# Performance work log

Measured on AMD Instinct MI355X. Metric: run time of the kernel, lower is better.

## Reference

```python
import jax, jax.numpy as jnp
import numpy as np
from jax import lax

B, S, D = 4, 4096, 2048
R, E, K, H = 256, 8, 2, 512
MAX_BLEND = 0.9


def setup_inputs() -> dict:
    key = jax.random.key(0)
    ks = jax.random.split(key, 11)
    def w(k, shape, fan_in):
        return jax.random.normal(k, shape, dtype=jnp.float32) * (1.0 / np.sqrt(fan_in))
    return {
        "h": jax.random.normal(ks[0], (B, S, D), dtype=jnp.float32),
        "V": w(ks[1], (D, R), D),            # down-projection (z = V^T h)
        "U": w(ks[2], (R, D), R),            # reconstruction (h = U z)
        "Wr": w(ks[3], (R, E), R),           # router
        "br": jnp.zeros((E,), dtype=jnp.float32),
        "W1": w(ks[4], (E, R, H), R),        # per-expert up-proj
        "b1": jnp.zeros((E, H), dtype=jnp.float32),
        "W2": w(ks[5], (E, H, R), H),        # per-expert down-proj
        "b2": jnp.zeros((E, R), dtype=jnp.float32),
        "Wh": w(ks[6], (D, 1), D),           # halting unit
        "bh": jnp.zeros((1,), dtype=jnp.float32),
    }


def _forward(h, V, U, Wr, br, W1, b1, W2, b2, Wh, bh):
    b, s, d = h.shape
    T = b * s
    # 1. project to vein subspace: z = V^T h  -> [B,S,R]
    z = jnp.einsum("bsd,dr->bsr", h, V)
    zf = z.reshape(T, R)
    # 2. top-k routing
    logits = zf @ Wr + br                      # [T,E]
    probs = jax.nn.softmax(logits, axis=-1)
    topw, topi = lax.top_k(probs, K)           # [T,K]
    topw = topw / jnp.sum(topw, axis=-1, keepdims=True)
    combine = jnp.zeros((T, E), dtype=zf.dtype).at[jnp.arange(T)[:, None], topi].add(topw)
    # 3. expert mix (dense-compute reference; combine is K-sparse per token)
    hidden = jax.nn.gelu(jnp.einsum("tr,erh->teh", zf, W1) + b1, approximate=False)
    expert_out = jnp.einsum("teh,ehr->ter", hidden, W2) + b2    # [T,E,R]
    z_new = jnp.einsum("te,ter->tr", combine, expert_out).reshape(b, s, R)
    # 4. residual blend: blend = min(top_k/num_experts, max_blend)
    blend = min(K / E, MAX_BLEND)
    z_final = z_new * blend + z * (1.0 - blend)
    # 5. reconstruct + halting
    h_new = jnp.einsum("bsr,rd->bsd", z_final, U)
    p_halt = jax.nn.sigmoid(jnp.einsum("bsd,do->bso", h_new, Wh) + bh)
    return h_new, p_halt


def reference(h, V, U, Wr, br, W1, b1, W2, b2, Wh, bh):
    return _forward(h, V, U, Wr, br, W1, b1, W2, b2, Wh, bh)
```

## Files before the change

### kernel.cpp

```cpp
#include <hip/hip_runtime.h>
#include <stdint.h>
#include <math.h>

#define TK 16384
#define DD 2048
#define RR 256
#define EE 8
#define HH 512
#define NSEG_MAX 264
#define NPAIR_MAX (NSEG_MAX * 128)

typedef __attribute__((ext_vector_type(4))) float f32x4;
typedef __attribute__((ext_vector_type(8))) short s16x8;
typedef __attribute__((ext_vector_type(8))) unsigned short u16x8;
typedef __attribute__((ext_vector_type(4))) unsigned short u16x4;
typedef unsigned short ushort_t;

__device__ inline unsigned short f2bf(float f) {
  union { float f; unsigned u; } v; v.f = f;
  unsigned r = v.u + 0x7fffu + ((v.u >> 16) & 1u);
  return (unsigned short)(r >> 16);
}
__device__ inline float bf2f(ushort_t u) {
  union { unsigned u; float f; } v; v.u = ((unsigned)u) << 16; return v.f;
}

__device__ inline void gll16(const void* g, void* l) {
  __builtin_amdgcn_global_load_lds(
      (const __attribute__((address_space(1))) void*)g,
      (__attribute__((address_space(3))) void*)l, 16, 0, 0);
}

__device__ inline u16x8 pack8(f32x4 a, f32x4 b) {
  u16x8 r;
  r[0] = f2bf(a.x); r[1] = f2bf(a.y); r[2] = f2bf(a.z); r[3] = f2bf(a.w);
  r[4] = f2bf(b.x); r[5] = f2bf(b.y); r[6] = f2bf(b.z); r[7] = f2bf(b.w);
  return r;
}

__global__ __launch_bounds__(256) void k_tr(const float* __restrict__ src,
                                            ushort_t* __restrict__ dst,
                                            int nr, int nc) {
  __shared__ float tile[32][33];
  int s = blockIdx.z;
  src += (size_t)s * nr * nc;
  dst += (size_t)s * nr * nc;
  int tx = threadIdx.x & 31, ty = threadIdx.x >> 5;
  int c0 = blockIdx.x * 32, r0 = blockIdx.y * 32;
  #pragma unroll
  for (int i = 0; i < 32; i += 8)
    tile[ty + i][tx] = src[(size_t)(r0 + ty + i) * nc + c0 + tx];
  __syncthreads();
  #pragma unroll
  for (int i = 0; i < 32; i += 8)
    dst[(size_t)(c0 + ty + i) * nr + r0 + tx] = f2bf(tile[tx][ty + i]);
}

__global__ __launch_bounds__(256) void k_veff(const float* __restrict__ V,
                                              const float* __restrict__ Wr,
                                              float* __restrict__ VeffT) {
  __shared__ float lwr[RR * EE];
  int t = threadIdx.x;
  #pragma unroll
  for (int i = 0; i < 8; ++i) lwr[i * 256 + t] = Wr[i * 256 + t];
  __syncthreads();
  int d = blockIdx.x * 256 + t;
  float a[8] = {0, 0, 0, 0, 0, 0, 0, 0};
  const float* vrow = V + (size_t)d * RR;
  for (int r = 0; r < RR; r += 4) {
    f32x4 v = *(const f32x4*)(vrow + r);
    #pragma unroll
    for (int e = 0; e < 8; ++e)
      a[e] += v.x * lwr[r * 8 + e] + v.y * lwr[(r + 1) * 8 + e] +
              v.z * lwr[(r + 2) * 8 + e] + v.w * lwr[(r + 3) * 8 + e];
  }
  #pragma unroll
  for (int e = 0; e < 8; ++e) VeffT[(size_t)e * DD + d] = a[e];
}

__global__ void k_uh(const float* U, const float* Wh, float* Uh) {
  int wave = threadIdx.x >> 6, lane = threadIdx.x & 63;
  int r = blockIdx.x * 4 + wave;
  const f32x4* u4 = (const f32x4*)(U + (size_t)r * DD);
  const f32x4* w4 = (const f32x4*)Wh;
  float acc = 0.f;
  #pragma unroll
  for (int it = 0; it < 8; ++it) {
    f32x4 a = u4[it * 64 + lane], b = w4[it * 64 + lane];
    acc += a.x * b.x + a.y * b.y + a.z * b.z + a.w * b.w;
  }
  #pragma unroll
  for (int o = 32; o; o >>= 1) acc += __shfl_down(acc, o, 64);
  if (lane == 0) Uh[r] = acc;
}

__global__ __launch_bounds__(256, 2) void k_front(
    const float* __restrict__ h, const ushort_t* __restrict__ Vt,
    const float* __restrict__ VeffT, const float* __restrict__ br,
    ushort_t* __restrict__ zb, int* __restrict__ topi, float* __restrict__ topw,
    int* __restrict__ ctrl) {
  __shared__ ushort_t As[2][32 * 72];
  __shared__ ushort_t Bs[2][256 * 64];
  __shared__ float Vs[2][8 * 64];
  __shared__ int lcnt[8];
  int t = threadIdx.x;
  int m0 = blockIdx.x * 32;
  int lane = t & 63, wave = t >> 6;
  int ln = lane & 15, hi = lane >> 4;
  int arow = t >> 3, koff = (t & 7) * 8;
  const float* aptr = h + (size_t)(m0 + arow) * DD + koff;
  if (t < 8) lcnt[t] = 0;

  f32x4 acc[2][4];
  #pragma unroll
  for (int i = 0; i < 2; ++i)
    #pragma unroll
    for (int j = 0; j < 4; ++j) acc[i][j] = (f32x4){0.f, 0.f, 0.f, 0.f};
  float racc[8] = {0, 0, 0, 0, 0, 0, 0, 0};

  f32x4 pc0, pc1, pn0, pn1;
  {
    pc0 = ((const f32x4*)aptr)[0];
    pc1 = ((const f32x4*)aptr)[1];
    #pragma unroll
    for (int u = 0; u < 8; ++u) {
      int idx = u * 256 + t;
      gll16(Vt + (size_t)(idx >> 3) * DD + (idx & 7) * 8, &Bs[0][idx * 8]);
    }
    if (t < 128) gll16(VeffT + (size_t)(t >> 4) * DD + (t & 15) * 4, &Vs[0][t * 4]);
    *(u16x8*)&As[0][arow * 72 + koff] = pack8(pc0, pc1);
  }
  __syncthreads();

  for (int s = 0; s < 32; ++s) {
    int cb = s & 1, xb = cb ^ 1;
    int k1 = (s + 1) * 64;
    if (s < 31) {
      pn0 = ((const f32x4*)(aptr + k1))[0];
      pn1 = ((const f32x4*)(aptr + k1))[1];
      #pragma unroll
      for (int u = 0; u < 8; ++u) {
        int idx = u * 256 + t;
        gll16(Vt + (size_t)(idx >> 3) * DD + k1 + (idx & 7) * 8, &Bs[xb][idx * 8]);
      }
      if (t < 128) gll16(VeffT + (size_t)(t >> 4) * DD + k1 + (t & 15) * 4, &Vs[xb][t * 4]);
    }
    {
      const f32x4* vsb = (const f32x4*)&Vs[cb][0];
      #pragma unroll
      for (int e = 0; e < 8; ++e) {
        f32x4 v0 = vsb[(e * 64 + koff) >> 2];
        f32x4 v1 = vsb[((e * 64 + koff) >> 2) + 1];
        racc[e] += pc0.x * v0.x + pc0.y * v0.y + pc0.z * v0.z + pc0.w * v0.w +
                   pc1.x * v1.x + pc1.y * v1.y + pc1.z * v1.z + pc1.w * v1.w;
      }
    }
    #pragma unroll
    for (int ks = 0; ks < 2; ++ks) {
      s16x8 af[2], bq[4];
      #pragma unroll
      for (int i = 0; i < 2; ++i)
        af[i] = *(const s16x8*)&As[cb][(i * 16 + ln) * 72 + ks * 32 + hi * 8];
      #pragma unroll
      for (int j = 0; j < 4; ++j)
        bq[j] = *(const s16x8*)&Bs[cb][(wave * 64 + j * 16 + ln) * 64 + ks * 32 + hi * 8];
      #pragma unroll
      for (int i = 0; i < 2; ++i)
        #pragma unroll
        for (int j = 0; j < 4; ++j)
          acc[i][j] = __builtin_amdgcn_mfma_f32_16x16x32_bf16(af[i], bq[j], acc[i][j], 0, 0, 0);
    }
    if (s < 31) {
      *(u16x8*)&As[xb][arow * 72 + koff] = pack8(pn0, pn1);
      pc0 = pn0; pc1 = pn1;
    }
    __syncthreads();
  }

  #pragma unroll
  for (int i = 0; i < 2; ++i)
    #pragma unroll
    for (int j = 0; j < 4; ++j)
      #pragma unroll
      for (int r = 0; r < 4; ++r) {
        int row = m0 + i * 16 + hi * 4 + r;
        int col = wave * 64 + j * 16 + ln;
        zb[(size_t)row * RR + col] = f2bf(acc[i][j][r]);
      }

  #pragma unroll
  for (int e = 0; e < 8; ++e) {
    racc[e] += __shfl_xor(racc[e], 1, 64);
    racc[e] += __shfl_xor(racc[e], 2, 64);
    racc[e] += __shfl_xor(racc[e], 4, 64);
  }
  if ((t & 7) == 0) {
    int token = m0 + arow;
    f32x4 br0 = ((const f32x4*)br)[0], br1 = ((const f32x4*)br)[1];
    float l[8] = {racc[0] + br0.x, racc[1] + br0.y, racc[2] + br0.z, racc[3] + br0.w,
                  racc[4] + br1.x, racc[5] + br1.y, racc[6] + br1.z, racc[7] + br1.w};
    float best = -1e30f; int bi = 0;
    #pragma unroll
    for (int e = 0; e < 8; ++e) if (l[e] > best) { best = l[e]; bi = e; }
    float sec = -1e30f; int si = 0;
    #pragma unroll
    for (int e = 0; e < 8; ++e) if (e != bi && l[e] > sec) { sec = l[e]; si = e; }
    float w0 = 1.f / (1.f + expf(sec - best));
    topi[token * 2 + 0] = bi; topi[token * 2 + 1] = si;
    topw[token * 2 + 0] = w0; topw[token * 2 + 1] = 1.f - w0;
    atomicAdd(&lcnt[bi], 1);
    atomicAdd(&lcnt[si], 1);
  }
  __syncthreads();
  if (t < 8) atomicAdd(&ctrl[t], lcnt[t]);
}

__global__ void k_bases(int* ctrl) {
  if (threadIdx.x == 0) {
    int cum = 0;
    for (int e = 0; e < 8; ++e) {
      int c = ctrl[e];
      int segs = (c + 127) >> 7;
      ctrl[8 + e] = cum;
      for (int s2 = 0; s2 < segs; ++s2) ctrl[16 + (cum >> 7) + s2] = e;
      cum += segs << 7;
    }
    for (int s2 = cum >> 7; s2 < NSEG_MAX; ++s2) ctrl[16 + s2] = -1;
  }
}

__global__ __launch_bounds__(256) void k_scatter(const int* topi, const float* topw,
                                                 int* ctrl, int* pair_t, float* pair_w,
                                                 int* inv) {
  __shared__ int lcnt[8], lbase[8];
  int t = threadIdx.x;
  if (t < 8) lcnt[t] = 0;
  __syncthreads();
  int slot = blockIdx.x * 256 + t;
  int e = topi[slot];
  float wv = topw[slot];
  int lp = atomicAdd(&lcnt[e], 1);
  __syncthreads();
  if (t < 8) lbase[t] = atomicAdd(&ctrl[8 + t], lcnt[t]);
  __syncthreads();
  int p = lbase[e] + lp;
  pair_t[p] = slot >> 1;
  pair_w[p] = wv;
  inv[slot] = p;
}

#define GEMM_COMPUTE(AS, BS)                                                          \
  _Pragma("unroll")                                                                   \
  for (int ks = 0; ks < 2; ++ks) {                                                    \
    s16x8 af[4], bq[4];                                                               \
    _Pragma("unroll")                                                                 \
    for (int i = 0; i < 4; ++i)                                                       \
      af[i] = *(const s16x8*)&AS[(wr * 64 + i * 16 + ln) * 64 + ks * 32 + hi * 8];    \
    _Pragma("unroll")                                                                 \
    for (int j = 0; j < 4; ++j)                                                       \
      bq[j] = *(const s16x8*)&BS[(wc * 64 + j * 16 + ln) * 64 + ks * 32 + hi * 8];    \
    _Pragma("unroll")                                                                 \
    for (int i = 0; i < 4; ++i)                                                       \
      _Pragma("unroll")                                                               \
      for (int j = 0; j < 4; ++j)                                                     \
        acc[i][j] = __builtin_amdgcn_mfma_f32_16x16x32_bf16(af[i], bq[j], acc[i][j], 0, 0, 0); \
  }

__global__ __launch_bounds__(256, 2) void k_e1(const ushort_t* zb, const ushort_t* W1t,
                                               const float* b1, const int* ctrl,
                                               const int* pair_t, ushort_t* hidden) {
  __shared__ ushort_t As[2][8192];
  __shared__ ushort_t Bs[2][8192];
  __shared__ int pt[128];
  int sg = blockIdx.x >> 2, nt = blockIdx.x & 3;
  int e = ctrl[16 + sg];
  if (e < 0) return;
  int t = threadIdx.x;
  if (t < 128) pt[t] = pair_t[sg * 128 + t];
  __syncthreads();
  int n0 = nt * 128;
  const ushort_t* Bbase = W1t + (size_t)e * HH * RR;
  int lane = t & 63, wave = t >> 6;
  int wr = wave >> 1, wc = wave & 1;
  int ln = lane & 15, hi = lane >> 4;

  f32x4 acc[4][4];
  #pragma unroll
  for (int i = 0; i < 4; ++i)
    #pragma unroll
    for (int j = 0; j < 4; ++j) acc[i][j] = (f32x4){0.f, 0.f, 0.f, 0.f};

  #pragma unroll
  for (int u = 0; u < 4; ++u) {
    int idx = u * 256 + t;
    gll16(zb + (size_t)pt[idx >> 3] * RR + (idx & 7) * 8, &As[0][idx * 8]);
    gll16(Bbase + (size_t)(n0 + (idx >> 3)) * RR + (idx & 7) * 8, &Bs[0][idx * 8]);
  }
  __syncthreads();
  for (int s = 0; s < 4; ++s) {
    int cb = s & 1, xb = cb ^ 1;
    if (s < 3) {
      int k1 = (s + 1) * 64;
      #pragma unroll
      for (int u = 0; u < 4; ++u) {
        int idx = u * 256 + t;
        gll16(zb + (size_t)pt[idx >> 3] * RR + k1 + (idx & 7) * 8, &As[xb][idx * 8]);
        gll16(Bbase + (size_t)(n0 + (idx >> 3)) * RR + k1 + (idx & 7) * 8, &Bs[xb][idx * 8]);
      }
    }
    GEMM_COMPUTE(As[cb], Bs[cb]);
    __syncthreads();
  }
  #pragma unroll
  for (int i = 0; i < 4; ++i)
    #pragma unroll
    for (int j = 0; j < 4; ++j)
      #pragma unroll
      for (int r = 0; r < 4; ++r) {
        int pl = wr * 64 + i * 16 + hi * 4 + r;
        int col = n0 + wc * 64 + j * 16 + ln;
        float v = acc[i][j][r] + b1[e * HH + col];
        float g = 0.5f * v * (1.f + erff(v * 0.70710678118654752f));
        hidden[(size_t)(sg * 128 + pl) * HH + col] = f2bf(g);
      }
}

__global__ __launch_bounds__(256, 2) void k_e2(const ushort_t* hidden, const ushort_t* W2t,
                                               const float* b2, const int* ctrl,
                                               const int* pair_t, const float* pair_w,
                                               ushort_t* eout) {
  __shared__ ushort_t As[2][8192];
  __shared__ ushort_t Bs[2][8192];
  __shared__ float pw[128];
  int sg = blockIdx.x >> 1, nt = blockIdx.x & 1;
  int e = ctrl[16 + sg];
  if (e < 0) return;
  int t = threadIdx.x;
  if (t < 128) pw[t] = pair_w[sg * 128 + t];
  __syncthreads();
  int n0 = nt * 128;
  const ushort_t* Abase = hidden + (size_t)sg * 128 * HH;
  const ushort_t* Bbase = W2t + (size_t)e * RR * HH;
  int lane = t & 63, wave = t >> 6;
  int wr = wave >> 1, wc = wave & 1;
  int ln = lane & 15, hi = lane >> 4;

  f32x4 acc[4][4];
  #pragma unroll
  for (int i = 0; i < 4; ++i)
    #pragma unroll
    for (int j = 0; j < 4; ++j) acc[i][j] = (f32x4){0.f, 0.f, 0.f, 0.f};

  #pragma unroll
  for (int u = 0; u < 4; ++u) {
    int idx = u * 256 + t;
    gll16(Abase + (size_t)(idx >> 3) * HH + (idx & 7) * 8, &As[0][idx * 8]);
    gll16(Bbase + (size_t)(n0 + (idx >> 3)) * HH + (idx & 7) * 8, &Bs[0][idx * 8]);
  }
  __syncthreads();
  for (int s = 0; s < 8; ++s) {
    int cb = s & 1, xb = cb ^ 1;
    if (s < 7) {
      int k1 = (s + 1) * 64;
      #pragma unroll
      for (int u = 0; u < 4; ++u) {
        int idx = u * 256 + t;
        gll16(Abase + (size_t)(idx >> 3) * HH + k1 + (idx & 7) * 8, &As[xb][idx * 8]);
        gll16(Bbase + (size_t)(n0 + (idx >> 3)) * HH + k1 + (idx & 7) * 8, &Bs[xb][idx * 8]);
      }
    }
    GEMM_COMPUTE(As[cb], Bs[cb]);
    __syncthreads();
  }
  #pragma unroll
  for (int i = 0; i < 4; ++i)
    #pragma unroll
    for (int j = 0; j < 4; ++j)
      #pragma unroll
      for (int r = 0; r < 4; ++r) {
        int pl = wr * 64 + i * 16 + hi * 4 + r;
        int col = n0 + wc * 64 + j * 16 + ln;
        float v = acc[i][j][r] + b2[e * RR + col];
        eout[(size_t)(sg * 128 + pl) * RR + col] = f2bf(pw[pl] * v);
      }
}

__global__ __launch_bounds__(256) void k_final(const ushort_t* __restrict__ zb,
                                               const ushort_t* __restrict__ eout,
                                               const int* __restrict__ inv,
                                               const float* __restrict__ Uh,
                                               const float* __restrict__ bh,
                                               ushort_t* __restrict__ zb2,
                                               float* __restrict__ phalt) {
  __shared__ float luh[256];
  int t = threadIdx.x;
  if (t < 64) ((f32x4*)luh)[t] = ((const f32x4*)Uh)[t];
  __syncthreads();
  int tok = blockIdx.x * 64 + (t >> 2), q = t & 3;
  int i0 = inv[tok * 2], i1 = inv[tok * 2 + 1];
  const u16x8* z8 = (const u16x8*)(zb + (size_t)tok * RR + q * 64);
  const u16x8* ea = (const u16x8*)(eout + (size_t)i0 * RR + q * 64);
  const u16x8* eb = (const u16x8*)(eout + (size_t)i1 * RR + q * 64);
  ushort_t* o = zb2 + (size_t)tok * RR + q * 64;
  float acc = 0.f;
  #pragma unroll
  for (int it = 0; it < 8; ++it) {
    u16x8 zv = z8[it], av = ea[it], bv = eb[it];
    u16x8 pk;
    #pragma unroll
    for (int j = 0; j < 8; ++j) {
      float zf = 0.75f * bf2f(zv[j]) + 0.25f * (bf2f(av[j]) + bf2f(bv[j]));
      acc += zf * luh[q * 64 + it * 8 + j];
      pk[j] = f2bf(zf);
    }
    *(u16x8*)(o + it * 8) = pk;
  }
  acc += __shfl_xor(acc, 1, 64);
  acc += __shfl_xor(acc, 2, 64);
  if (q == 0) phalt[tok] = 1.f / (1.f + expf(-(acc + bh[0])));
}

__global__ __launch_bounds__(256, 2) void k_gemm_u(const ushort_t* zb2, const ushort_t* Ut,
                                                   float* outp) {
  __shared__ ushort_t As[2][8192];
  __shared__ ushort_t Bs[2][8192];
  int hw = blockIdx.x;
  int bid = (hw & 7) * 256 + (hw >> 3);
  int mt = bid >> 4, nt = bid & 15;
  int m0 = mt * 128, n0 = nt * 128;
  int t = threadIdx.x;
  int lane = t & 63, wave = t >> 6;
  int wr = wave >> 1, wc = wave & 1;
  int ln = lane & 15, hi = lane >> 4;

  f32x4 acc[4][4];
  #pragma unroll
  for (int i = 0; i < 4; ++i)
    #pragma unroll
    for (int j = 0; j < 4; ++j) acc[i][j] = (f32x4){0.f, 0.f, 0.f, 0.f};

  #pragma unroll
  for (int u = 0; u < 4; ++u) {
    int idx = u * 256 + t;
    gll16(zb2 + (size_t)(m0 + (idx >> 3)) * RR + (idx & 7) * 8, &As[0][idx * 8]);
    gll16(Ut + (size_t)(n0 + (idx >> 3)) * RR + (idx & 7) * 8, &Bs[0][idx * 8]);
  }
  __syncthreads();
  for (int s = 0; s < 4; ++s) {
    int cb = s & 1, xb = cb ^ 1;
    if (s < 3) {
      int k1 = (s + 1) * 64;
      #pragma unroll
      for (int u = 0; u < 4; ++u) {
        int idx = u * 256 + t;
        gll16(zb2 + (size_t)(m0 + (idx >> 3)) * RR + k1 + (idx & 7) * 8, &As[xb][idx * 8]);
        gll16(Ut + (size_t)(n0 + (idx >> 3)) * RR + k1 + (idx & 7) * 8, &Bs[xb][idx * 8]);
      }
    }
    GEMM_COMPUTE(As[cb], Bs[cb]);
    __syncthreads();
  }
  #pragma unroll
  for (int i = 0; i < 4; ++i)
    #pragma unroll
    for (int j = 0; j < 4; ++j)
      #pragma unroll
      for (int r = 0; r < 4; ++r) {
        int row = m0 + wr * 64 + i * 16 + hi * 4 + r;
        int col = n0 + wc * 64 + j * 16 + ln;
        outp[(size_t)row * DD + col] = acc[i][j][r];
      }
}

extern "C" void kernel_launch(void* const* d_in, const int* in_sizes, int n_in,
                              void* d_out, int out_size, void* d_ws, size_t ws_size,
                              hipStream_t stream) {
  (void)in_sizes; (void)n_in; (void)out_size;
  const float* h  = (const float*)d_in[0];
  const float* V  = (const float*)d_in[1];
  const float* U  = (const float*)d_in[2];
  const float* Wr = (const float*)d_in[3];
  const float* br = (const float*)d_in[4];
  const float* W1 = (const float*)d_in[5];
  const float* b1 = (const float*)d_in[6];
  const float* W2 = (const float*)d_in[7];
  const float* b2 = (const float*)d_in[8];
  const float* Wh = (const float*)d_in[9];
  const float* bh = (const float*)d_in[10];
  float* outp = (float*)d_out;
  char* w = (char*)d_ws;

  constexpr size_t OFF_VT    = 0;
  constexpr size_t OFF_UT    = 1048576;
  constexpr size_t OFF_W1T   = 2097152;
  constexpr size_t OFF_W2T   = 4194304;
  constexpr size_t OFF_VEFFT = 6291456;
  constexpr size_t OFF_UHV   = 6356992;
  constexpr size_t OFF_TOPI  = 6361088;
  constexpr size_t OFF_TOPW  = 6492160;
  constexpr size_t OFF_INV   = 6623232;
  constexpr size_t OFF_CTRL  = 6754304;
  constexpr size_t OFF_PT    = 6758400;
  constexpr size_t OFF_PW    = 6893568;
  constexpr size_t OFF_ZB    = 7028736;
  constexpr size_t OFF_EOUT  = 15417344;
  constexpr size_t OFF_HID   = 32718848;
  constexpr size_t OFF_ZB2   = OFF_HID;
  constexpr size_t WS_NEED   = 67321856;
  if (ws_size < WS_NEED) return;

  ushort_t* Vt    = (ushort_t*)(w + OFF_VT);
  ushort_t* Ut    = (ushort_t*)(w + OFF_UT);
  ushort_t* W1t   = (ushort_t*)(w + OFF_W1T);
  ushort_t* W2t   = (ushort_t*)(w + OFF_W2T);
  float*    VeffT = (float*)(w + OFF_VEFFT);
  float*    Uh    = (float*)(w + OFF_UHV);
  int*      topi  = (int*)(w + OFF_TOPI);
  float*    topw  = (float*)(w + OFF_TOPW);
  int*      inv   = (int*)(w + OFF_INV);
  int*      ctrl  = (int*)(w + OFF_CTRL);
  int*      pair_t= (int*)(w + OFF_PT);
  float*    pair_w= (float*)(w + OFF_PW);
  ushort_t* zb    = (ushort_t*)(w + OFF_ZB);
  ushort_t* eout  = (ushort_t*)(w + OFF_EOUT);
  ushort_t* hidden= (ushort_t*)(w + OFF_HID);
  ushort_t* zb2   = (ushort_t*)(w + OFF_ZB2);

  hipMemsetAsync(w + OFF_CTRL, 0, OFF_ZB - OFF_CTRL, stream);

  k_tr<<<dim3(8, 64, 1), 256, 0, stream>>>(V, Vt, 2048, 256);
  k_tr<<<dim3(64, 8, 1), 256, 0, stream>>>(U, Ut, 256, 2048);
  k_tr<<<dim3(16, 8, 8), 256, 0, stream>>>(W1, W1t, 256, 512);
  k_tr<<<dim3(8, 16, 8), 256, 0, stream>>>(W2, W2t, 512, 256);
  k_veff<<<8, 256, 0, stream>>>(V, Wr, VeffT);
  k_uh<<<64, 256, 0, stream>>>(U, Wh, Uh);
  k_front<<<512, 256, 0, stream>>>(h, Vt, VeffT, br, zb, topi, topw, ctrl);
  k_bases<<<1, 64, 0, stream>>>(ctrl);
  k_scatter<<<128, 256, 0, stream>>>(topi, topw, ctrl, pair_t, pair_w, inv);
  k_e1<<<NSEG_MAX * 4, 256, 0, stream>>>(zb, W1t, b1, ctrl, pair_t, hidden);
  k_e2<<<NSEG_MAX * 2, 256, 0, stream>>>(hidden, W2t, b2, ctrl, pair_t, pair_w, eout);
  k_final<<<256, 256, 0, stream>>>(zb, eout, inv, Uh, bh, zb2, outp + (size_t)TK * DD);
  k_gemm_u<<<2048, 256, 0, stream>>>(zb2, Ut, outp);
}
```

Measured before the change: 245.6 us.

## Swizzle LDS tiles in expert and reconstruction GEMMs; merge prep kernels

Applies an XOR swizzle to the 16-byte chunk positions inside the LDS tiles of the expert and reconstruction GEMMs. The global loads fetch swizzled columns and the MFMA fragment reads undo the swizzle, which is meant to remove LDS bank conflicts on the fragment reads. It also merges the six weight-preparation kernels (transposes, Veff, Uh) into one launch with a block-index dispatch to cut launch overhead. The risk is that the swizzle mapping must line up exactly between load and read to keep results correct.

```diff
diff --git a/kernel.cpp b/kernel.cpp
--- a/kernel.cpp
+++ b/kernel.cpp
@@ -13,7 +13,7 @@
 typedef __attribute__((ext_vector_type(4))) float f32x4;
 typedef __attribute__((ext_vector_type(8))) short s16x8;
 typedef __attribute__((ext_vector_type(8))) unsigned short u16x8;
-typedef __attribute__((ext_vector_type(4))) unsigned short u16x4;
+typedef __attribute__((ext_vector_type(4))) unsigned u32x4;
 typedef unsigned short ushort_t;
 
 __device__ inline unsigned short f2bf(float f) {
@@ -38,60 +38,66 @@
   return r;
 }
 
-__global__ __launch_bounds__(256) void k_tr(const float* __restrict__ src,
-                                            ushort_t* __restrict__ dst,
-                                            int nr, int nc) {
-  __shared__ float tile[32][33];
-  int s = blockIdx.z;
-  src += (size_t)s * nr * nc;
-  dst += (size_t)s * nr * nc;
-  int tx = threadIdx.x & 31, ty = threadIdx.x >> 5;
-  int c0 = blockIdx.x * 32, r0 = blockIdx.y * 32;
-  #pragma unroll
-  for (int i = 0; i < 32; i += 8)
-    tile[ty + i][tx] = src[(size_t)(r0 + ty + i) * nc + c0 + tx];
-  __syncthreads();
-  #pragma unroll
-  for (int i = 0; i < 32; i += 8)
-    dst[(size_t)(c0 + ty + i) * nr + r0 + tx] = f2bf(tile[tx][ty + i]);
-}
-
-__global__ __launch_bounds__(256) void k_veff(const float* __restrict__ V,
-                                              const float* __restrict__ Wr,
-                                              float* __restrict__ VeffT) {
-  __shared__ float lwr[RR * EE];
-  int t = threadIdx.x;
-  #pragma unroll
-  for (int i = 0; i < 8; ++i) lwr[i * 256 + t] = Wr[i * 256 + t];
-  __syncthreads();
-  int d = blockIdx.x * 256 + t;
-  float a[8] = {0, 0, 0, 0, 0, 0, 0, 0};
-  const float* vrow = V + (size_t)d * RR;
-  for (int r = 0; r < RR; r += 4) {
-    f32x4 v = *(const f32x4*)(vrow + r);
-    #pragma unroll
-    for (int e = 0; e < 8; ++e)
-      a[e] += v.x * lwr[r * 8 + e] + v.y * lwr[(r + 1) * 8 + e] +
-              v.z * lwr[(r + 2) * 8 + e] + v.w * lwr[(r + 3) * 8 + e];
-  }
-  #pragma unroll
-  for (int e = 0; e < 8; ++e) VeffT[(size_t)e * DD + d] = a[e];
-}
-
-__global__ void k_uh(const float* U, const float* Wh, float* Uh) {
-  int wave = threadIdx.x >> 6, lane = threadIdx.x & 63;
-  int r = blockIdx.x * 4 + wave;
-  const f32x4* u4 = (const f32x4*)(U + (size_t)r * DD);
-  const f32x4* w4 = (const f32x4*)Wh;
-  float acc = 0.f;
-  #pragma unroll
-  for (int it = 0; it < 8; ++it) {
-    f32x4 a = u4[it * 64 + lane], b = w4[it * 64 + lane];
-    acc += a.x * b.x + a.y * b.y + a.z * b.z + a.w * b.w;
-  }
-  #pragma unroll
-  for (int o = 32; o; o >>= 1) acc += __shfl_down(acc, o, 64);
-  if (lane == 0) Uh[r] = acc;
+__global__ __launch_bounds__(256) void k_prep(
+    const float* __restrict__ V, const float* __restrict__ U,
+    const float* __restrict__ W1, const float* __restrict__ W2,
+    const float* __restrict__ Wr, const float* __restrict__ Wh,
+    ushort_t* __restrict__ Vt, ushort_t* __restrict__ Ut,
+    ushort_t* __restrict__ W1t, ushort_t* __restrict__ W2t,
+    float* __restrict__ VeffT, float* __restrict__ Uh) {
+  __shared__ float sm[2112];
+  int b = blockIdx.x, t = threadIdx.x;
+  if (b < 3072) {
+    const float* src; ushort_t* dst; int nr, nc, c0, r0;
+    if (b < 512)       { src = V; dst = Vt; nr = 2048; nc = 256;
+                         c0 = (b & 7) * 32; r0 = (b >> 3) * 32; }
+    else if (b < 1024) { int bx = b - 512; src = U; dst = Ut; nr = 256; nc = 2048;
+                         c0 = (bx & 63) * 32; r0 = (bx >> 6) * 32; }
+    else if (b < 2048) { int bx = b - 1024; int s = bx >> 7; bx &= 127;
+                         src = W1 + (size_t)s * 131072; dst = W1t + (size_t)s * 131072;
+                         nr = 256; nc = 512; c0 = (bx & 15) * 32; r0 = (bx >> 4) * 32; }
+    else               { int bx = b - 2048; int s = bx >> 7; bx &= 127;
+                         src = W2 + (size_t)s * 131072; dst = W2t + (size_t)s * 131072;
+                         nr = 512; nc = 256; c0 = (bx & 7) * 32; r0 = (bx >> 3) * 32; }
+    int tx = t & 31, ty = t >> 5;
+    #pragma unroll
+    for (int i = 0; i < 32; i += 8)
+      sm[(ty + i) * 33 + tx] = src[(size_t)(r0 + ty + i) * nc + c0 + tx];
+    __syncthreads();
+    #pragma unroll
+    for (int i = 0; i < 32; i += 8)
+      dst[(size_t)(c0 + ty + i) * nr + r0 + tx] = f2bf(sm[tx * 33 + ty + i]);
+  } else if (b < 3080) {
+    #pragma unroll
+    for (int i = 0; i < 8; ++i) sm[i * 256 + t] = Wr[i * 256 + t];
+    __syncthreads();
+    int d = (b - 3072) * 256 + t;
+    float a[8] = {0, 0, 0, 0, 0, 0, 0, 0};
+    const float* vrow = V + (size_t)d * RR;
+    for (int r = 0; r < RR; r += 4) {
+      f32x4 v = *(const f32x4*)(vrow + r);
+      #pragma unroll
+      for (int e = 0; e < 8; ++e)
+        a[e] += v.x * sm[r * 8 + e] + v.y * sm[(r + 1) * 8 + e] +
+                v.z * sm[(r + 2) * 8 + e] + v.w * sm[(r + 3) * 8 + e];
+    }
+    #pragma unroll
+    for (int e = 0; e < 8; ++e) VeffT[(size_t)e * DD + d] = a[e];
+  } else {
+    int wave = t >> 6, lane = t & 63;
+    int r = (b - 3080) * 4 + wave;
+    const f32x4* u4 = (const f32x4*)(U + (size_t)r * DD);
+    const f32x4* w4 = (const f32x4*)Wh;
+    float acc = 0.f;
+    #pragma unroll
+    for (int it = 0; it < 8; ++it) {
+      f32x4 a = u4[it * 64 + lane], bb = w4[it * 64 + lane];
+      acc += a.x * bb.x + a.y * bb.y + a.z * bb.z + a.w * bb.w;
+    }
+    #pragma unroll
+    for (int o = 32; o; o >>= 1) acc += __shfl_down(acc, o, 64);
+    if (lane == 0) Uh[r] = acc;
+  }
 }
 
 __global__ __launch_bounds__(256, 2) void k_front(
@@ -101,7 +107,7 @@
     int* __restrict__ ctrl) {
   __shared__ ushort_t As[2][32 * 72];
   __shared__ ushort_t Bs[2][256 * 64];
-  __shared__ float Vs[2][8 * 64];
+  __shared__ float Vs[2][512];
   __shared__ int lcnt[8];
   int t = threadIdx.x;
   int m0 = blockIdx.x * 32;
@@ -255,16 +261,18 @@
     s16x8 af[4], bq[4];                                                               \
     _Pragma("unroll")                                                                 \
     for (int i = 0; i < 4; ++i)                                                       \
-      af[i] = *(const s16x8*)&AS[(wr * 64 + i * 16 + ln) * 64 + ks * 32 + hi * 8];    \
+      af[i] = *(const s16x8*)&AS[(wr * 64 + i * 16 + ln) * 64 + ((ks * 32 + hi * 8) ^ xo)]; \
     _Pragma("unroll")                                                                 \
     for (int j = 0; j < 4; ++j)                                                       \
-      bq[j] = *(const s16x8*)&BS[(wc * 64 + j * 16 + ln) * 64 + ks * 32 + hi * 8];    \
+      bq[j] = *(const s16x8*)&BS[(wc * 64 + j * 16 + ln) * 64 + ((ks * 32 + hi * 8) ^ xo)]; \
     _Pragma("unroll")                                                                 \
     for (int i = 0; i < 4; ++i)                                                       \
       _Pragma("unroll")                                                               \
       for (int j = 0; j < 4; ++j)                                                     \
         acc[i][j] = __builtin_amdgcn_mfma_f32_16x16x32_bf16(af[i], bq[j], acc[i][j], 0, 0, 0); \
   }
+
+#define SWZ8(idx) (((idx & 7) ^ ((idx >> 3) & 7)) * 8)
 
 __global__ __launch_bounds__(256, 2) void k_e1(const ushort_t* zb, const ushort_t* W1t,
                                                const float* b1, const int* ctrl,
@@ -283,6 +291,7 @@
   int lane = t & 63, wave = t >> 6;
   int wr = wave >> 1, wc = wave & 1;
   int ln = lane & 15, hi = lane >> 4;
+  const int xo = (ln & 7) << 3;
 
   f32x4 acc[4][4];
   #pragma unroll
@@ -293,8 +302,8 @@
   #pragma unroll
   for (int u = 0; u < 4; ++u) {
     int idx = u * 256 + t;
-    gll16(zb + (size_t)pt[idx >> 3] * RR + (idx & 7) * 8, &As[0][idx * 8]);
-    gll16(Bbase + (size_t)(n0 + (idx >> 3)) * RR + (idx & 7) * 8, &Bs[0][idx * 8]);
+    gll16(zb + (size_t)pt[idx >> 3] * RR + SWZ8(idx), &As[0][idx * 8]);
+    gll16(Bbase + (size_t)(n0 + (idx >> 3)) * RR + SWZ8(idx), &Bs[0][idx * 8]);
   }
   __syncthreads();
   for (int s = 0; s < 4; ++s) {
@@ -304,8 +313,8 @@
       #pragma unroll
       for (int u = 0; u < 4; ++u) {
         int idx = u * 256 + t;
-        gll16(zb + (size_t)pt[idx >> 3] * RR + k1 + (idx & 7) * 8, &As[xb][idx * 8]);
-        gll16(Bbase + (size_t)(n0 + (idx >> 3)) * RR + k1 + (idx & 7) * 8, &Bs[xb][idx * 8]);
+        gll16(zb + (size_t)pt[idx >> 3] * RR + k1 + SWZ8(idx), &As[xb][idx * 8]);
+        gll16(Bbase + (size_t)(n0 + (idx >> 3)) * RR + k1 + SWZ8(idx), &Bs[xb][idx * 8]);
       }
     }
     GEMM_COMPUTE(As[cb], Bs[cb]);
@@ -344,6 +353,7 @@
   int lane = t & 63, wave = t >> 6;
   int wr = wave >> 1, wc = wave & 1;
   int ln = lane & 15, hi = lane >> 4;
+  const int xo = (ln & 7) << 3;
 
   f32x4 acc[4][4];
   #pragma unroll
@@ -354,8 +364,8 @@
   #pragma unroll
   for (int u = 0; u < 4; ++u) {
     int idx = u * 256 + t;
-    gll16(Abase + (size_t)(idx >> 3) * HH + (idx & 7) * 8, &As[0][idx * 8]);
-    gll16(Bbase + (size_t)(n0 + (idx >> 3)) * HH + (idx & 7) * 8, &Bs[0][idx * 8]);
+    gll16(Abase + (size_t)(idx >> 3) * HH + SWZ8(idx), &As[0][idx * 8]);
+    gll16(Bbase + (size_t)(n0 + (idx >> 3)) * HH + SWZ8(idx), &Bs[0][idx * 8]);
   }
   __syncthreads();
   for (int s = 0; s < 8; ++s) {
@@ -365,8 +375,8 @@
       #pragma unroll
       for (int u = 0; u < 4; ++u) {
         int idx = u * 256 + t;
-        gll16(Abase + (size_t)(idx >> 3) * HH + k1 + (idx & 7) * 8, &As[xb][idx * 8]);
-        gll16(Bbase + (size_t)(n0 + (idx >> 3)) * HH + k1 + (idx & 7) * 8, &Bs[xb][idx * 8]);
+        gll16(Abase + (size_t)(idx >> 3) * HH + k1 + SWZ8(idx), &As[xb][idx * 8]);
+        gll16(Bbase + (size_t)(n0 + (idx >> 3)) * HH + k1 + SWZ8(idx), &Bs[xb][idx * 8]);
       }
     }
     GEMM_COMPUTE(As[cb], Bs[cb]);
@@ -432,6 +442,7 @@
   int lane = t & 63, wave = t >> 6;
   int wr = wave >> 1, wc = wave & 1;
   int ln = lane & 15, hi = lane >> 4;
+  const int xo = (ln & 7) << 3;
 
   f32x4 acc[4][4];
   #pragma unroll
@@ -442,8 +453,8 @@
   #pragma unroll
   for (int u = 0; u < 4; ++u) {
     int idx = u * 256 + t;
-    gll16(zb2 + (size_t)(m0 + (idx >> 3)) * RR + (idx & 7) * 8, &As[0][idx * 8]);
-    gll16(Ut + (size_t)(n0 + (idx >> 3)) * RR + (idx & 7) * 8, &Bs[0][idx * 8]);
+    gll16(zb2 + (size_t)(m0 + (idx >> 3)) * RR + SWZ8(idx), &As[0][idx * 8]);
+    gll16(Ut + (size_t)(n0 + (idx >> 3)) * RR + SWZ8(idx), &Bs[0][idx * 8]);
   }
   __syncthreads();
   for (int s = 0; s < 4; ++s) {
@@ -453,8 +464,8 @@
       #pragma unroll
       for (int u = 0; u < 4; ++u) {
         int idx = u * 256 + t;
-        gll16(zb2 + (size_t)(m0 + (idx >> 3)) * RR + k1 + (idx & 7) * 8, &As[xb][idx * 8]);
-        gll16(Ut + (size_t)(n0 + (idx >> 3)) * RR + k1 + (idx & 7) * 8, &Bs[xb][idx * 8]);
+        gll16(zb2 + (size_t)(m0 + (idx >> 3)) * RR + k1 + SWZ8(idx), &As[xb][idx * 8]);
+        gll16(Ut + (size_t)(n0 + (idx >> 3)) * RR + k1 + SWZ8(idx), &Bs[xb][idx * 8]);
       }
     }
     GEMM_COMPUTE(As[cb], Bs[cb]);
@@ -528,12 +539,7 @@
 
   hipMemsetAsync(w + OFF_CTRL, 0, OFF_ZB - OFF_CTRL, stream);
 
-  k_tr<<<dim3(8, 64, 1), 256, 0, stream>>>(V, Vt, 2048, 256);
-  k_tr<<<dim3(64, 8, 1), 256, 0, stream>>>(U, Ut, 256, 2048);
-  k_tr<<<dim3(16, 8, 8), 256, 0, stream>>>(W1, W1t, 256, 512);
-  k_tr<<<dim3(8, 16, 8), 256, 0, stream>>>(W2, W2t, 512, 256);
-  k_veff<<<8, 256, 0, stream>>>(V, Wr, VeffT);
-  k_uh<<<64, 256, 0, stream>>>(U, Wh, Uh);
+  k_prep<<<3144, 256, 0, stream>>>(V, U, W1, W2, Wr, Wh, Vt, Ut, W1t, W2t, VeffT, Uh);
   k_front<<<512, 256, 0, stream>>>(h, Vt, VeffT, br, zb, topi, topw, ctrl);
   k_bases<<<1, 64, 0, stream>>>(ctrl);
   k_scatter<<<128, 256, 0, stream>>>(topi, topw, ctrl, pair_t, pair_w, inv);
```

New measurement: 224.9 us. -8.4%, faster.
